# Kernel tuning notes

Measured on AMD Instinct MI355X. Metric: run time of the kernel, lower is better.

## Reference

```python
import jax, jax.numpy as jnp
import numpy as np

B, N, M, T = 120, 128, 192, 25
PHI_MIN, PHI_MAX = 1e-6, 30.0


def _phi(x):
    # phi(x) = -log(tanh(x/2)); self-inverse map used for exact sum-product CN update
    return -jnp.log(jnp.tanh(0.5 * jnp.clip(x, PHI_MIN, PHI_MAX)))


def setup_inputs() -> dict:
    rng = np.random.default_rng(0)
    Hx = (rng.random((M, N)) < 4.0 / N).astype(np.float32)   # weight-4 stabilizer-like rows
    Hz = (rng.random((M, N)) < 4.0 / N).astype(np.float32)
    Gx = (rng.random((2, N)) < 16.0 / N).astype(np.float32)  # logical checks for the loss
    Gz = (rng.random((2, N)) < 16.0 / N).astype(np.float32)
    errorx = (rng.random((B, N)) < 0.05).astype(np.float32)  # X-component indicator
    errorz = (rng.random((B, N)) < 0.05).astype(np.float32)  # Z-component indicator
    return {
        "errorx": jnp.asarray(errorx),
        "errorz": jnp.asarray(errorz),
        "ep0": jnp.full((1,), 0.1, jnp.float32),
        "Hx": jnp.asarray(Hx),
        "Hz": jnp.asarray(Hz),
        "Gx": jnp.asarray(Gx),
        "Gz": jnp.asarray(Gz),
        "weights_llr": jnp.ones((T,), jnp.float32),
        "weights_vn": jnp.ones((T,), jnp.float32),
        "weights_cn": jnp.ones((T,), jnp.float32),
    }


def reference(errorx, errorz, ep0, Hx, Hz, Gx, Gz, weights_llr, weights_vn, weights_cn):
    ep = ep0[0]
    # depolarizing channel LLR: P(X-component) = 2*ep/3
    llr0 = jnp.log((1.0 - 2.0 * ep / 3.0) / (2.0 * ep / 3.0))
    Hs = jnp.stack([Hz, Hx])                                   # (2,M,N): ch0 detects X errors, ch1 Z
    synx = jnp.remainder(errorx @ Hz.T, 2.0)                   # (B,M)
    synz = jnp.remainder(errorz @ Hx.T, 2.0)
    syn_sign = 1.0 - 2.0 * jnp.stack([synx, synz], axis=1)     # (B,2,M)
    HALF_PI = jnp.float32(np.pi / 2)

    def iter_loss(Gamma):
        # loss of eq. 11: soft corrections must reproduce a zero syndrome on G
        prob = jax.nn.sigmoid(-Gamma)
        pX, pZ = prob[:, 0, :], prob[:, 1, :]
        corrz = jnp.where(errorz > 0.5, 1.0 - pX, pX)          # qz/qy -> 1-pX, qx/qi -> pX
        corrx = jnp.where(errorx > 0.5, 1.0 - pZ, pZ)
        sx = jnp.einsum('gn,bn->bg', Gz, corrx)
        sz = jnp.einsum('gn,bn->bg', Gx, corrz)
        return (jnp.sum(jnp.abs(jnp.sin(HALF_PI * sz)), axis=1)
                + jnp.sum(jnp.abs(jnp.sin(HALF_PI * sx)), axis=1))

    def body(V, w):
        w_llr, w_vn, w_cn = w
        # --- check node update (exact box-plus via sign/phi decomposition) ---
        sgn = jnp.where(Hs > 0, jnp.where(V < 0, -1.0, 1.0), 1.0)
        tot_sgn = jnp.prod(sgn, axis=3, keepdims=True)         # (B,2,M,1)
        p = jnp.where(Hs > 0, _phi(jnp.abs(V)), 0.0)
        p_sum = jnp.sum(p, axis=3, keepdims=True)
        cn = syn_sign[..., None] * tot_sgn * sgn * _phi(p_sum - p) * Hs * w_cn
        # --- variable node update ---
        cn_sum = jnp.sum(cn, axis=2)                           # (B,2,N)
        Gamma = w_llr * llr0 + cn_sum                          # (B,2,N) marginal LLRs
        Vnew = (w_llr * llr0 + w_vn * (cn_sum[:, :, None, :] - cn)) * Hs
        return Vnew, iter_loss(Gamma)

    V0 = jnp.broadcast_to(llr0 * Hs, (errorx.shape[0], 2, Hs.shape[1], Hs.shape[2]))
    _, losses = jax.lax.scan(body, V0, (weights_llr, weights_vn, weights_cn))  # (T,B)
    loss = jnp.mean(jnp.sum(losses, axis=0))
    loss_min = jnp.mean(jnp.min(losses, axis=0))
    return jnp.stack([loss, loss_min])
```

## Files before the change

kernel.cpp:

```cpp
#include <hip/hip_runtime.h>
#include <math.h>

#define Bsz 120
#define Nv  128
#define Ms  192
#define Tit 25
#define EPAD 1024
#define KE4 4
#define DC  16
#define DV  24

#define WS_CNT  0
#define WS_PART 2

__device__ __forceinline__ float phi_f(float x) {
  x = fminf(fmaxf(x, 1e-6f), 30.0f);
  const float u = __expf(-x);
  float den = 1.0f - u;
  if (x < 0.03125f) den = x * (1.0f - 0.5f * x + 0.16666667f * x * x);
  return 0.69314718f * (__log2f(1.0f + u) - __log2f(den));
}

#define USH(arr, k) ((arr[(k) >> 1] >> (((k) & 1) * 16)) & 0xffff)

__global__ __launch_bounds__(256, 1) void nbp_kernel(
    const float* __restrict__ errorx, const float* __restrict__ errorz,
    const float* __restrict__ ep0,
    const float* __restrict__ Hx, const float* __restrict__ Hz,
    const float* __restrict__ Gx, const float* __restrict__ Gz,
    const float* __restrict__ w_llr, const float* __restrict__ w_vn,
    const float* __restrict__ w_cn,
    int* __restrict__ W, float* __restrict__ out) {
  __shared__ unsigned mask_l[Ms][4];
  __shared__ int rp_l[Ms + 1];
  __shared__ unsigned colmask[Nv][6];
  __shared__ unsigned char vcol8[EPAD];
  __shared__ unsigned char echk8[EPAD];
  __shared__ unsigned short veid_l[Nv * DV];
  __shared__ float p_l[EPAD + 1];
  __shared__ float cn_l[EPAD + 1];
  __shared__ float csum_l[Nv + 1];
  __shared__ float2 pt2[256];
  __shared__ float corrbuf[2][Nv];
  __shared__ float wls[Tit], wvs[Tit], wcs[Tit];
  __shared__ int wtot[3];
  __shared__ float wred[4], wredm[4];
  __shared__ int lastFlag;

  const int tid = threadIdx.x;
  const int lane = tid & 63, wv = tid >> 6;
  const int bid = blockIdx.x;
  const int b = bid >> 1, s = bid & 1;
  float* partBase = (float*)(W + WS_PART);
  float* part = partBase + (s * Bsz + b) * Tit;

  const float ep   = ep0[0];
  const float a23  = (2.0f * ep) / 3.0f;
  const float llr0 = logf((1.0f - a23) / a23);

  if (tid < Tit) {
    wls[tid] = w_llr[tid];
    wvs[tid] = w_vn[tid];
    wcs[tid] = w_cn[tid];
  }
  {
    unsigned* cmf = &colmask[0][0];
    for (int i = tid; i < Nv * 6; i += 256) cmf[i] = 0;
    unsigned* v32 = (unsigned*)veid_l;
    for (int i = tid; i < Nv * DV / 2; i += 256) v32[i] = (EPAD << 16) | EPAD;
  }
  unsigned mwa[4] = {0, 0, 0, 0};
  int d = 0;
  if (tid < Ms) {
    const float4* H4 = (const float4*)((s ? Hx : Hz) + tid * Nv);
#pragma unroll
    for (int w = 0; w < 4; ++w) {
      unsigned bits = 0;
#pragma unroll
      for (int q = 0; q < 8; ++q) {
        const float4 v = H4[w * 8 + q];
        if (v.x > 0.f) bits |= 1u << (q * 4 + 0);
        if (v.y > 0.f) bits |= 1u << (q * 4 + 1);
        if (v.z > 0.f) bits |= 1u << (q * 4 + 2);
        if (v.w > 0.f) bits |= 1u << (q * 4 + 3);
      }
      mwa[w] = bits;
      mask_l[tid][w] = bits;
      d += __popc(bits);
    }
  }
  __syncthreads();

  {
    int x = d;
#pragma unroll
    for (int off = 1; off < 64; off <<= 1) {
      const int y = __shfl_up(x, off);
      if (lane >= off) x += y;
    }
    if (lane == 63 && wv < 3) wtot[wv] = x;
    __syncthreads();
    int carry = 0;
    for (int k = 0; k < wv && k < 3; ++k) carry += wtot[k];
    if (tid < Ms) {
      const int incl = x + carry;
      rp_l[tid] = incl - d;
      if (tid == Ms - 1) rp_l[Ms] = incl;
    }
  }
  __syncthreads();
  const int E = rp_l[Ms];

  if (tid < Ms) {
    int o = rp_l[tid];
    const unsigned wbit = 1u << (tid & 31);
    const int wrd = tid >> 5;
#pragma unroll
    for (int w = 0; w < 4; ++w) {
      unsigned bits = mwa[w];
      while (bits) {
        const int j = __ffs(bits) - 1;
        bits &= bits - 1;
        const int n = w * 32 + j;
        if (o < EPAD) { vcol8[o] = (unsigned char)n; echk8[o] = (unsigned char)tid; }
        atomicOr(&colmask[n][wrd], wbit);
        ++o;
      }
    }
  }
  for (int e = E + tid; e < EPAD; e += 256) {
    vcol8[e] = (unsigned char)Nv;
    echk8[e] = (unsigned char)Ms;
  }
  if (tid < Nv) {
    const float* esyn = (s ? errorz : errorx) + b * Nv;
    csum_l[tid] = esyn[tid];
  }
  if (tid == 0) {
    csum_l[Nv] = 0.f;
    p_l[EPAD] = 0.f;
    cn_l[EPAD] = 0.f;
  }
  __syncthreads();

  unsigned vcolp[2] = {0, 0}, chkp[2] = {0, 0};
#pragma unroll
  for (int k = 0; k < KE4; ++k) {
    const int e = tid + (k << 8);
    vcolp[k >> 1] |= ((unsigned)vcol8[e]) << ((k & 1) * 16);
    chkp[k >> 1]  |= ((unsigned)echk8[e]) << ((k & 1) * 16);
  }
  int rp0 = 0, dg0 = 0;
  if (tid < Ms) {
    rp0 = rp_l[tid];
    const int dd = rp_l[tid + 1] - rp0;
    dg0 = (dd <= DC) ? dd : DC;
  }
  if (tid < Nv) {
    const int wnd = tid >> 5;
    const unsigned lowmask = (1u << (tid & 31)) - 1u;
    int kk = 0;
#pragma unroll
    for (int w6 = 0; w6 < 6; ++w6) {
      unsigned bits = colmask[tid][w6];
      while (bits) {
        const int m2 = w6 * 32 + (__ffs(bits) - 1);
        bits &= bits - 1;
        int r = __popc(mask_l[m2][wnd] & lowmask);
        for (int w = 0; w < wnd; ++w) r += __popc(mask_l[m2][w]);
        if (kk < DV) veid_l[tid * DV + kk] = (unsigned short)(rp_l[m2] + r);
        ++kk;
      }
    }
  }
#pragma unroll
  for (int k = 0; k < KE4; ++k) {
    const int e = tid + (k << 8);
    const int nn = USH(vcolp, k);
    p_l[e] = (csum_l[nn] > 0.5f) ? -1.f : 1.f;
  }
  const int l2 = tid - 128;
  float g0a = 0.f, g0b = 0.f, g1a = 0.f, g1b = 0.f;
  if (tid >= 128 && tid < 192) {
    const float* G = s ? Gz : Gx;
    g0a = G[l2]; g0b = G[l2 + 64];
    g1a = G[Nv + l2]; g1b = G[Nv + l2 + 64];
  }
  float ec = 0.f;
  if (tid < Nv) ec = ((s ? errorx : errorz) + b * Nv)[tid];
  __syncthreads();

  unsigned vep[12];
  if (tid < Nv) {
    const uint4* q = (const uint4*)(veid_l + tid * DV);
    const uint4 a0 = q[0], a1 = q[1], a2 = q[2];
    vep[0] = a0.x; vep[1] = a0.y; vep[2]  = a0.z; vep[3]  = a0.w;
    vep[4] = a1.x; vep[5] = a1.y; vep[6]  = a1.z; vep[7]  = a1.w;
    vep[8] = a2.x; vep[9] = a2.y; vep[10] = a2.z; vep[11] = a2.w;
  } else {
#pragma unroll
    for (int i = 0; i < 12; ++i) vep[i] = (EPAD << 16) | EPAD;
  }
  float ssgn;
  {
    unsigned par = 0;
#pragma unroll
    for (int k = 0; k < DC; ++k) {
      const int addr = (k < dg0) ? (rp0 + k) : EPAD;
      par ^= __float_as_uint(p_l[addr]) >> 31;
    }
    ssgn = (par & 1u) ? -1.f : 1.f;
  }
  __syncthreads();

  float cn_reg[KE4] = {0.f, 0.f, 0.f, 0.f};
  float basePrev = llr0, wvPrev = 0.f;

#pragma unroll 1
  for (int t = 0; t < Tit; ++t) {
    const float wct = wcs[t];

    float pe[KE4];
#pragma unroll
    for (int k = 0; k < KE4; ++k) {
      const int e = tid + (k << 8);
      const int nn = USH(vcolp, k);
      const float csv = csum_l[nn];
      const float Vk = basePrev + wvPrev * (csv - cn_reg[k]);
      float pv = phi_f(fabsf(Vk));
      pv = fmaxf(pv, 1e-30f);
      pv = (Vk < 0.f) ? -pv : pv;
      pe[k] = pv;
      p_l[e] = pv;
    }
    __syncthreads();

    {
      float psum = 0.f;
      unsigned par = 0;
#pragma unroll
      for (int k = 0; k < DC; ++k) {
        const int addr = (k < dg0) ? (rp0 + k) : EPAD;
        const float v = p_l[addr];
        par ^= __float_as_uint(v) >> 31;
        psum += fabsf(v);
      }
      const float tt = ((par & 1u) ? -ssgn : ssgn) * wct;
      pt2[tid] = make_float2(psum, tt);
    }
    __syncthreads();

#pragma unroll
    for (int k = 0; k < KE4; ++k) {
      const int cc = USH(chkp, k);
      const float2 q = pt2[cc];
      const float ps = pe[k];
      const float sg = (__float_as_uint(ps) >> 31) ? -1.f : 1.f;
      const float cnk = q.y * sg * phi_f(q.x - fabsf(ps));
      cn_reg[k] = cnk;
      cn_l[tid + (k << 8)] = cnk;
    }
    __syncthreads();

    const float base_t = wls[t] * llr0;
    if (tid < Nv) {
      float cs = 0.f;
#pragma unroll
      for (int k = 0; k < DV; ++k) cs += cn_l[USH(vep, k)];
      csum_l[tid] = cs;
      const float prob = 1.0f / (1.0f + __expf(base_t + cs));
      corrbuf[t & 1][tid] = (ec > 0.5f) ? 1.0f - prob : prob;
    } else if (tid < 192 && t > 0) {
      const float* cr = corrbuf[(t - 1) & 1];
      const float c0 = cr[l2], c1 = cr[l2 + 64];
      float la = g0a * c0 + g0b * c1;
      float lb = g1a * c0 + g1b * c1;
#pragma unroll
      for (int off = 1; off < 64; off <<= 1) {
        la += __shfl_xor(la, off);
        lb += __shfl_xor(lb, off);
      }
      const float lt = fabsf(__sinf(1.57079632679f * la)) +
                       fabsf(__sinf(1.57079632679f * lb));
      if (l2 == 0) part[t - 1] = lt;
    }
    basePrev = base_t;
    wvPrev = wvs[t];
    __syncthreads();
  }

  if (tid >= 128 && tid < 192) {
    const float* cr = corrbuf[(Tit - 1) & 1];
    const float c0 = cr[l2], c1 = cr[l2 + 64];
    float la = g0a * c0 + g0b * c1;
    float lb = g1a * c0 + g1b * c1;
#pragma unroll
    for (int off = 1; off < 64; off <<= 1) {
      la += __shfl_xor(la, off);
      lb += __shfl_xor(lb, off);
    }
    const float lt = fabsf(__sinf(1.57079632679f * la)) +
                     fabsf(__sinf(1.57079632679f * lb));
    if (l2 == 0) part[Tit - 1] = lt;
  }
  __syncthreads();

  __threadfence();
  if (tid == 0) lastFlag = (atomicAdd(W + WS_CNT, 1) == 2 * Bsz - 1);
  __syncthreads();
  if (lastFlag) {
    __threadfence();
    float sm = 0.f, mn = 0.f;
    if (tid < Bsz) {
      const float* pa = partBase + tid * Tit;
      const float* pb = partBase + (Bsz + tid) * Tit;
      float acc = 0.f, mloc = 3.0e38f;
#pragma unroll
      for (int t = 0; t < Tit; ++t) {
        const float lt = pa[t] + pb[t];
        acc += lt;
        mloc = fminf(mloc, lt);
      }
      sm = acc;
      mn = mloc;
    }
#pragma unroll
    for (int off = 32; off; off >>= 1) {
      sm += __shfl_down(sm, off);
      mn += __shfl_down(mn, off);
    }
    if ((tid & 63) == 0) { wred[tid >> 6] = sm; wredm[tid >> 6] = mn; }
    __syncthreads();
    if (tid == 0) {
      out[0] = (wred[0] + wred[1]) * (1.0f / Bsz);
      out[1] = (wredm[0] + wredm[1]) * (1.0f / Bsz);
    }
  }
}

extern "C" void kernel_launch(void* const* d_in, const int* in_sizes, int n_in,
                              void* d_out, int out_size, void* d_ws, size_t ws_size,
                              hipStream_t stream) {
  const float* errorx = (const float*)d_in[0];
  const float* errorz = (const float*)d_in[1];
  const float* ep0    = (const float*)d_in[2];
  const float* Hx     = (const float*)d_in[3];
  const float* Hz     = (const float*)d_in[4];
  const float* Gx     = (const float*)d_in[5];
  const float* Gz     = (const float*)d_in[6];
  const float* wllr   = (const float*)d_in[7];
  const float* wvn    = (const float*)d_in[8];
  const float* wcn    = (const float*)d_in[9];
  float* out = (float*)d_out;
  int* W = (int*)d_ws;

  hipMemsetAsync((void*)(W + WS_CNT), 0, sizeof(int), stream);
  hipLaunchKernelGGL(nbp_kernel, dim3(2 * Bsz), dim3(256), 0, stream,
                     errorx, errorz, ep0, Hx, Hz, Gx, Gz, wllr, wvn, wcn, W, out);
}
```

Baseline: 133.9 us.

## Fuse check-node phi and extrinsic into per-check threads; defer loss computation

```diff
diff --git a/kernel.cpp b/kernel.cpp
--- a/kernel.cpp
+++ b/kernel.cpp
@@ -5,10 +5,11 @@
 #define Nv  128
 #define Ms  192
 #define Tit 25
-#define EPAD 1024
-#define KE4 4
 #define DC  16
 #define DV  24
+#define EPADW 960
+#define SENT  1152
+#define CNSZ  1153
 
 #define WS_CNT  0
 #define WS_PART 2
@@ -34,15 +35,13 @@
   __shared__ unsigned mask_l[Ms][4];
   __shared__ int rp_l[Ms + 1];
   __shared__ unsigned colmask[Nv][6];
-  __shared__ unsigned char vcol8[EPAD];
-  __shared__ unsigned char echk8[EPAD];
+  __shared__ unsigned short ncol_l[Ms * DC];
   __shared__ unsigned short veid_l[Nv * DV];
-  __shared__ float p_l[EPAD + 1];
-  __shared__ float cn_l[EPAD + 1];
+  __shared__ float cn_l[CNSZ];
   __shared__ float csum_l[Nv + 1];
-  __shared__ float2 pt2[256];
-  __shared__ float corrbuf[2][Nv];
+  __shared__ float corrh[Tit][Nv];
   __shared__ float wls[Tit], wvs[Tit], wcs[Tit];
+  __shared__ float plost[Tit];
   __shared__ int wtot[3];
   __shared__ float wred[4], wredm[4];
   __shared__ int lastFlag;
@@ -66,9 +65,15 @@
   {
     unsigned* cmf = &colmask[0][0];
     for (int i = tid; i < Nv * 6; i += 256) cmf[i] = 0;
-    unsigned* v32 = (unsigned*)veid_l;
-    for (int i = tid; i < Nv * DV / 2; i += 256) v32[i] = (EPAD << 16) | EPAD;
-  }
+    unsigned* nc32 = (unsigned*)ncol_l;
+    for (int i = tid; i < Ms * DC / 2; i += 256) nc32[i] = (Nv << 16) | Nv;
+    for (int i = tid; i < CNSZ; i += 256) cn_l[i] = 0.f;
+  }
+  if (tid < Nv) {
+    const float* esyn = (s ? errorz : errorx) + b * Nv;
+    csum_l[tid] = esyn[tid];
+  }
+  if (tid == 0) csum_l[Nv] = 0.f;
   unsigned mwa[4] = {0, 0, 0, 0};
   int d = 0;
   if (tid < Ms) {
@@ -89,10 +94,11 @@
       d += __popc(bits);
     }
   }
+  const int dgc = (d <= DC) ? d : DC;
   __syncthreads();
 
   {
-    int x = d;
+    int x = dgc;
 #pragma unroll
     for (int off = 1; off < 64; off <<= 1) {
       const int y = __shfl_up(x, off);
@@ -104,17 +110,16 @@
     for (int k = 0; k < wv && k < 3; ++k) carry += wtot[k];
     if (tid < Ms) {
       const int incl = x + carry;
-      rp_l[tid] = incl - d;
+      rp_l[tid] = incl - dgc;
       if (tid == Ms - 1) rp_l[Ms] = incl;
     }
   }
   __syncthreads();
-  const int E = rp_l[Ms];
 
   if (tid < Ms) {
-    int o = rp_l[tid];
     const unsigned wbit = 1u << (tid & 31);
     const int wrd = tid >> 5;
+    int cnt = 0;
 #pragma unroll
     for (int w = 0; w < 4; ++w) {
       unsigned bits = mwa[w];
@@ -122,40 +127,23 @@
         const int j = __ffs(bits) - 1;
         bits &= bits - 1;
         const int n = w * 32 + j;
-        if (o < EPAD) { vcol8[o] = (unsigned char)n; echk8[o] = (unsigned char)tid; }
+        if (cnt < DC) ncol_l[tid * DC + cnt] = (unsigned short)n;
+        ++cnt;
         atomicOr(&colmask[n][wrd], wbit);
-        ++o;
-      }
-    }
-  }
-  for (int e = E + tid; e < EPAD; e += 256) {
-    vcol8[e] = (unsigned char)Nv;
-    echk8[e] = (unsigned char)Ms;
-  }
-  if (tid < Nv) {
-    const float* esyn = (s ? errorz : errorx) + b * Nv;
-    csum_l[tid] = esyn[tid];
-  }
-  if (tid == 0) {
-    csum_l[Nv] = 0.f;
-    p_l[EPAD] = 0.f;
-    cn_l[EPAD] = 0.f;
-  }
-  __syncthreads();
-
-  unsigned vcolp[2] = {0, 0}, chkp[2] = {0, 0};
-#pragma unroll
-  for (int k = 0; k < KE4; ++k) {
-    const int e = tid + (k << 8);
-    vcolp[k >> 1] |= ((unsigned)vcol8[e]) << ((k & 1) * 16);
-    chkp[k >> 1]  |= ((unsigned)echk8[e]) << ((k & 1) * 16);
-  }
-  int rp0 = 0, dg0 = 0;
-  if (tid < Ms) {
-    rp0 = rp_l[tid];
-    const int dd = rp_l[tid + 1] - rp0;
-    dg0 = (dd <= DC) ? dd : DC;
-  }
+      }
+    }
+  }
+  __syncthreads();
+
+  unsigned ncp[8];
+  {
+    const uint4* q = (const uint4*)(ncol_l + ((tid < Ms) ? tid : 0) * DC);
+    const uint4 a0 = q[0], a1 = q[1];
+    ncp[0] = a0.x; ncp[1] = a0.y; ncp[2] = a0.z; ncp[3] = a0.w;
+    ncp[4] = a1.x; ncp[5] = a1.y; ncp[6] = a1.z; ncp[7] = a1.w;
+  }
+  const int rp0 = (tid < Ms) ? rp_l[tid] : 0;
+  const int dg0 = (tid < Ms) ? dgc : 0;
   if (tid < Nv) {
     const int wnd = tid >> 5;
     const unsigned lowmask = (1u << (tid & 31)) - 1u;
@@ -168,28 +156,28 @@
         bits &= bits - 1;
         int r = __popc(mask_l[m2][wnd] & lowmask);
         for (int w = 0; w < wnd; ++w) r += __popc(mask_l[m2][w]);
-        if (kk < DV) veid_l[tid * DV + kk] = (unsigned short)(rp_l[m2] + r);
-        ++kk;
-      }
-    }
-  }
-#pragma unroll
-  for (int k = 0; k < KE4; ++k) {
-    const int e = tid + (k << 8);
-    const int nn = USH(vcolp, k);
-    p_l[e] = (csum_l[nn] > 0.5f) ? -1.f : 1.f;
-  }
-  const int l2 = tid - 128;
-  float g0a = 0.f, g0b = 0.f, g1a = 0.f, g1b = 0.f;
-  if (tid >= 128 && tid < 192) {
-    const float* G = s ? Gz : Gx;
-    g0a = G[l2]; g0b = G[l2 + 64];
-    g1a = G[Nv + l2]; g1b = G[Nv + l2 + 64];
-  }
+        if (kk < DV && r < DC) veid_l[tid * DV + kk] = (unsigned short)(rp_l[m2] + r);
+        if (r < DC) ++kk;
+      }
+    }
+    for (int z = kk; z < DV; ++z) veid_l[tid * DV + z] = (unsigned short)SENT;
+  }
+  float ssgn;
+  {
+    unsigned par = 0;
+#pragma unroll
+    for (int k = 0; k < DC; ++k) {
+      const int nn = USH(ncp, k);
+      const float ev = csum_l[nn];
+      par ^= (k < dg0) ? ((ev > 0.5f) ? 1u : 0u) : 0u;
+    }
+    ssgn = (par & 1u) ? -1.f : 1.f;
+  }
+  const float* G = s ? Gz : Gx;
+  const float g0a = G[lane],      g0b = G[lane + 64];
+  const float g1a = G[Nv + lane], g1b = G[Nv + lane + 64];
   float ec = 0.f;
   if (tid < Nv) ec = ((s ? errorx : errorz) + b * Nv)[tid];
-  __syncthreads();
-
   unsigned vep[12];
   if (tid < Nv) {
     const uint4* q = (const uint4*)(veid_l + tid * DV);
@@ -199,66 +187,42 @@
     vep[8] = a2.x; vep[9] = a2.y; vep[10] = a2.z; vep[11] = a2.w;
   } else {
 #pragma unroll
-    for (int i = 0; i < 12; ++i) vep[i] = (EPAD << 16) | EPAD;
-  }
-  float ssgn;
-  {
-    unsigned par = 0;
-#pragma unroll
-    for (int k = 0; k < DC; ++k) {
-      const int addr = (k < dg0) ? (rp0 + k) : EPAD;
-      par ^= __float_as_uint(p_l[addr]) >> 31;
-    }
-    ssgn = (par & 1u) ? -1.f : 1.f;
-  }
-  __syncthreads();
-
-  float cn_reg[KE4] = {0.f, 0.f, 0.f, 0.f};
+    for (int i = 0; i < 12; ++i) vep[i] = (SENT << 16) | SENT;
+  }
+  __syncthreads();
+
+  float cn_reg[DC];
+#pragma unroll
+  for (int k = 0; k < DC; ++k) cn_reg[k] = 0.f;
   float basePrev = llr0, wvPrev = 0.f;
 
 #pragma unroll 1
   for (int t = 0; t < Tit; ++t) {
-    const float wct = wcs[t];
-
-    float pe[KE4];
-#pragma unroll
-    for (int k = 0; k < KE4; ++k) {
-      const int e = tid + (k << 8);
-      const int nn = USH(vcolp, k);
-      const float csv = csum_l[nn];
-      const float Vk = basePrev + wvPrev * (csv - cn_reg[k]);
-      float pv = phi_f(fabsf(Vk));
-      pv = fmaxf(pv, 1e-30f);
-      pv = (Vk < 0.f) ? -pv : pv;
-      pe[k] = pv;
-      p_l[e] = pv;
-    }
-    __syncthreads();
-
-    {
+    if (tid < Ms) {
+      const float wct = wcs[t];
+      float pa[DC];
       float psum = 0.f;
       unsigned par = 0;
 #pragma unroll
       for (int k = 0; k < DC; ++k) {
-        const int addr = (k < dg0) ? (rp0 + k) : EPAD;
-        const float v = p_l[addr];
-        par ^= __float_as_uint(v) >> 31;
-        psum += fabsf(v);
-      }
-      const float tt = ((par & 1u) ? -ssgn : ssgn) * wct;
-      pt2[tid] = make_float2(psum, tt);
-    }
-    __syncthreads();
-
-#pragma unroll
-    for (int k = 0; k < KE4; ++k) {
-      const int cc = USH(chkp, k);
-      const float2 q = pt2[cc];
-      const float ps = pe[k];
-      const float sg = (__float_as_uint(ps) >> 31) ? -1.f : 1.f;
-      const float cnk = q.y * sg * phi_f(q.x - fabsf(ps));
-      cn_reg[k] = cnk;
-      cn_l[tid + (k << 8)] = cnk;
+        const int nn = USH(ncp, k);
+        const float csv = csum_l[nn];
+        const float Vk = basePrev + wvPrev * (csv - cn_reg[k]);
+        const float pv = phi_f(fabsf(Vk));
+        pa[k] = (Vk < 0.f) ? -pv : pv;
+        psum += (k < dg0) ? pv : 0.f;
+        par ^= (k < dg0) ? (__float_as_uint(Vk) >> 31) : 0u;
+      }
+      const float tot = ((par & 1u) ? -ssgn : ssgn) * wct;
+#pragma unroll
+      for (int k = 0; k < DC; ++k) {
+        const float ps = pa[k];
+        const float sg = (__float_as_uint(ps) >> 31) ? -1.f : 1.f;
+        const float cnk = tot * sg * phi_f(psum - fabsf(ps));
+        cn_reg[k] = cnk;
+        const int addr = (k < dg0) ? (rp0 + k) : (EPADW + tid);
+        cn_l[addr] = cnk;
+      }
     }
     __syncthreads();
 
@@ -269,10 +233,18 @@
       for (int k = 0; k < DV; ++k) cs += cn_l[USH(vep, k)];
       csum_l[tid] = cs;
       const float prob = 1.0f / (1.0f + __expf(base_t + cs));
-      corrbuf[t & 1][tid] = (ec > 0.5f) ? 1.0f - prob : prob;
-    } else if (tid < 192 && t > 0) {
-      const float* cr = corrbuf[(t - 1) & 1];
-      const float c0 = cr[l2], c1 = cr[l2 + 64];
+      corrh[t][tid] = (ec > 0.5f) ? 1.0f - prob : prob;
+    }
+    basePrev = base_t;
+    wvPrev = wvs[t];
+    __syncthreads();
+  }
+
+#pragma unroll 1
+  for (int i = 0; i < 7; ++i) {
+    const int t = wv + 4 * i;
+    if (t < Tit) {
+      const float c0 = corrh[t][lane], c1 = corrh[t][lane + 64];
       float la = g0a * c0 + g0b * c1;
       float lb = g1a * c0 + g1b * c1;
 #pragma unroll
@@ -282,28 +254,12 @@
       }
       const float lt = fabsf(__sinf(1.57079632679f * la)) +
                        fabsf(__sinf(1.57079632679f * lb));
-      if (l2 == 0) part[t - 1] = lt;
-    }
-    basePrev = base_t;
-    wvPrev = wvs[t];
-    __syncthreads();
-  }
-
-  if (tid >= 128 && tid < 192) {
-    const float* cr = corrbuf[(Tit - 1) & 1];
-    const float c0 = cr[l2], c1 = cr[l2 + 64];
-    float la = g0a * c0 + g0b * c1;
-    float lb = g1a * c0 + g1b * c1;
-#pragma unroll
-    for (int off = 1; off < 64; off <<= 1) {
-      la += __shfl_xor(la, off);
-      lb += __shfl_xor(lb, off);
-    }
-    const float lt = fabsf(__sinf(1.57079632679f * la)) +
-                     fabsf(__sinf(1.57079632679f * lb));
-    if (l2 == 0) part[Tit - 1] = lt;
-  }
-  __syncthreads();
+      if (lane == 0) plost[t] = lt;
+    }
+  }
+  __syncthreads();
+
+  if (tid < Tit) part[tid] = plost[tid];
 
   __threadfence();
   if (tid == 0) lastFlag = (atomicAdd(W + WS_CNT, 1) == 2 * Bsz - 1);
@@ -312,12 +268,12 @@
     __threadfence();
     float sm = 0.f, mn = 0.f;
     if (tid < Bsz) {
-      const float* pa = partBase + tid * Tit;
-      const float* pb = partBase + (Bsz + tid) * Tit;
+      const float* pa2 = partBase + tid * Tit;
+      const float* pb2 = partBase + (Bsz + tid) * Tit;
       float acc = 0.f, mloc = 3.0e38f;
 #pragma unroll
       for (int t = 0; t < Tit; ++t) {
-        const float lt = pa[t] + pb[t];
+        const float lt = pa2[t] + pb2[t];
         acc += lt;
         mloc = fminf(mloc, lt);
       }
```

Result: slower. 151.6 us (+13.2%).
